# Kernel tuning notes

Hardware: AMD Instinct MI355X
Metric: run time of the kernel (lower is better)

The kernel has to match this reference:

```python
import jax, jax.numpy as jnp
import numpy as np

B, N, H, HEADS = 4, 4096, 256, 8
DEG = 16
E = B * N * DEG  # 262144 edges
DH = H // HEADS


def setup_inputs() -> dict:
    key = jax.random.key(0)
    ks = jax.random.split(key, 8)
    node_states = jax.random.normal(ks[0], (B, N, H), dtype=jnp.float32)
    # edge_indices rows: [batch_idx, target_node, source_node]
    b_idx = jnp.repeat(jnp.arange(B, dtype=jnp.int64), N * DEG)
    tgt = jnp.tile(jnp.repeat(jnp.arange(N, dtype=jnp.int64), DEG), B)
    src = jax.random.randint(ks[1], (E,), 0, N, dtype=jnp.int64)
    edge_indices = jnp.stack([b_idx, tgt, src])  # (3, E)
    s = 1.0 / np.sqrt(H)
    Wq = jax.random.normal(ks[2], (H, H), dtype=jnp.float32) * s
    Wk = jax.random.normal(ks[3], (H, H), dtype=jnp.float32) * s
    Wv = jax.random.normal(ks[4], (H, H), dtype=jnp.float32) * s
    bq = jnp.zeros((H,), dtype=jnp.float32)
    bk = jnp.zeros((H,), dtype=jnp.float32)
    bv = jnp.zeros((H,), dtype=jnp.float32)
    return {"node_states": node_states, "edge_indices": edge_indices,
            "Wq": Wq, "bq": bq, "Wk": Wk, "bk": bk, "Wv": Wv, "bv": bv}


def reference(node_states, edge_indices, Wq, bq, Wk, bk, Wv, bv):
    batch, n_nodes, hidden = node_states.shape
    b_idx, tgt, src = edge_indices[0], edge_indices[1], edge_indices[2]
    num_edges = b_idx.shape[0]

    # Dense Q/K/V projections on nodes (cheap), then per-edge gathers.
    Q = (node_states @ Wq + bq).reshape(batch, n_nodes, HEADS, DH)
    K = (node_states @ Wk + bk).reshape(batch, n_nodes, HEADS, DH)
    V = (node_states @ Wv + bv).reshape(batch, n_nodes, HEADS, DH)

    q_e = Q[b_idx, tgt]  # (E, heads, dh)
    k_e = K[b_idx, src]  # (E, heads, dh)
    scores = jnp.sum(q_e * k_e, axis=-1) / jnp.sqrt(jnp.float32(DH))  # (E, heads)

    # Segment softmax over source nodes, grouped per (batch, target) --
    # mirrors torch.sparse.softmax(logits, dim=-2).
    seg = b_idx * n_nodes + tgt  # (E,)
    num_seg = batch * n_nodes
    m = jax.ops.segment_max(scores, seg, num_segments=num_seg)  # (B*N, heads)
    exp = jnp.exp(scores - m[seg])
    denom = jax.ops.segment_sum(exp, seg, num_segments=num_seg)
    attn = exp / denom[seg]  # (E, heads)

    # Weighted scatter-sum of source values into target nodes
    # (replaces sparse edge_mask @ elwise_prod).
    v_e = V[b_idx, src]  # (E, heads, dh)
    weighted = (attn[..., None] * v_e).reshape(num_edges, hidden)
    out = jax.ops.segment_sum(weighted, seg, num_segments=num_seg)
    return out.reshape(batch, n_nodes, hidden)
```

## Files before the change

kernel.cpp:

```cpp
#include <hip/hip_runtime.h>
#include <hip/hip_bf16.h>

#define BATCH 4
#define NNODES 4096
#define HID 256
#define NHEADS 8
#define DH 32
#define DEG 16
#define NEDGES (BATCH * NNODES * DEG)
#define NROWS (BATCH * NNODES)

typedef __attribute__((ext_vector_type(8))) short short8;
typedef __attribute__((ext_vector_type(8))) unsigned short ushort8;
typedef __attribute__((ext_vector_type(4))) unsigned short u16x4;
typedef __attribute__((ext_vector_type(4))) float f32x4;

static __device__ __forceinline__ unsigned short f2bf(float f) {
  __hip_bfloat16 h = __float2bfloat16(f);
  return *reinterpret_cast<unsigned short*>(&h);
}
static __device__ __forceinline__ float bf2f(unsigned short u) {
  unsigned int v = ((unsigned int)u) << 16;
  return *reinterpret_cast<float*>(&v);
}

#define XBLOCKS 2048
#define WBLOCKS 96
__global__ __launch_bounds__(256) void prep_kernel(
    const float* __restrict__ X,
    const float* __restrict__ Wq, const float* __restrict__ Wk,
    const float* __restrict__ Wv,
    unsigned short* __restrict__ Xb, unsigned short* __restrict__ Wt) {
  const int tid = threadIdx.x;
  if (blockIdx.x < XBLOCKS) {
    const size_t base = (size_t)blockIdx.x * 2048 + (size_t)tid * 8;
    const float4 a = *reinterpret_cast<const float4*>(&X[base]);
    const float4 b = *reinterpret_cast<const float4*>(&X[base + 4]);
    ushort8 o;
    o[0] = f2bf(a.x); o[1] = f2bf(a.y); o[2] = f2bf(a.z); o[3] = f2bf(a.w);
    o[4] = f2bf(b.x); o[5] = f2bf(b.y); o[6] = f2bf(b.z); o[7] = f2bf(b.w);
    *reinterpret_cast<ushort8*>(&Xb[base]) = o;
  } else {
    const int o = (blockIdx.x - XBLOCKS) * 2048 + tid * 8;
    const int mat   = o >> 16;
    const int w     = o & 65535;
    const int strip = w >> 14;
    const int r     = w & 16383;
    const int kk    = r >> 11;
    const int hi    = (r >> 9) & 3;
    const int col   = (r >> 3) & 63;
    const int k0    = kk * 32 + hi * 8;
    const int c     = strip * 64 + col;
    const float* __restrict__ W = (mat == 0) ? Wq : (mat == 1) ? Wk : Wv;
    ushort8 ovec;
    #pragma unroll
    for (int j = 0; j < 8; ++j) {
      ovec[j] = f2bf(W[(size_t)(k0 + j) * HID + c]);
    }
    *reinterpret_cast<ushort8*>(&Wt[o]) = ovec;
  }
}

__global__ __launch_bounds__(256, 4) void qkv_mfma_kernel(
    const unsigned short* __restrict__ Xb, const unsigned short* __restrict__ Wt,
    const float* __restrict__ bq, const float* __restrict__ bk,
    const float* __restrict__ bv,
    float* __restrict__ Qs, unsigned short* __restrict__ Kb,
    unsigned short* __restrict__ Vb) {
  __shared__ unsigned short sW[16384];

  const int tid = threadIdx.x;
  const int s = blockIdx.x >> 8;
  const int chunk = blockIdx.x & 255;
  const int mat = s >> 2;
  const int c0 = (s & 3) * 64;

  const unsigned short* __restrict__ Wsrc = Wt + (size_t)(mat * 4 + (s & 3)) * 16384;
  #pragma unroll
  for (int i = 0; i < 8; ++i) {
    const int e = i * 2048 + tid * 8;
    *reinterpret_cast<ushort8*>(&sW[e]) =
        *reinterpret_cast<const ushort8*>(&Wsrc[e]);
  }

  const int lane = tid & 63;
  const int wv = tid >> 6;
  const int lm = lane & 15;
  const int hi = lane >> 4;
  const int lk = hi * 8;
  const int r0 = chunk * 64 + wv * 16;
  const int row = r0 + lm;

  short8 Af[8];
  #pragma unroll
  for (int kk = 0; kk < 8; ++kk) {
    Af[kk] = *reinterpret_cast<const short8*>(
        &Xb[(size_t)row * 256 + kk * 32 + lk]);
  }

  const float* __restrict__ bias = (mat == 0) ? bq : (mat == 1) ? bk : bv;

  __syncthreads();

  #pragma unroll
  for (int nt = 0; nt < 4; ++nt) {
    short8 Bf[8];
    #pragma unroll
    for (int kk = 0; kk < 8; ++kk) {
      Bf[kk] = *reinterpret_cast<const short8*>(
          &sW[kk * 2048 + hi * 512 + (nt * 16 + lm) * 8]);
    }
    f32x4 acc = {0.f, 0.f, 0.f, 0.f};
    #pragma unroll
    for (int kk = 0; kk < 8; ++kk) {
      acc = __builtin_amdgcn_mfma_f32_16x16x32_bf16(Bf[kk], Af[kk], acc, 0, 0, 0);
    }
    const int col0 = c0 + nt * 16 + hi * 4;
    const float4 b4 = *reinterpret_cast<const float4*>(&bias[col0]);
    if (mat == 0) {
      float4 o;
      o.x = acc[0] + b4.x; o.y = acc[1] + b4.y;
      o.z = acc[2] + b4.z; o.w = acc[3] + b4.w;
      *reinterpret_cast<float4*>(&Qs[(size_t)row * 256 + col0]) = o;
    } else {
      u16x4 o;
      o[0] = f2bf(acc[0] + b4.x); o[1] = f2bf(acc[1] + b4.y);
      o[2] = f2bf(acc[2] + b4.z); o[3] = f2bf(acc[3] + b4.w);
      unsigned short* __restrict__ dst = (mat == 1) ? Kb : Vb;
      *reinterpret_cast<u16x4*>(&dst[(size_t)row * 256 + col0]) = o;
    }
  }
}

__global__ __launch_bounds__(256) void attn_kernel(
    const float* __restrict__ Q, const unsigned short* __restrict__ K,
    const unsigned short* __restrict__ V, const int* __restrict__ edges,
    float* __restrict__ out) {
  __shared__ int s_n[DEG];
  __shared__ float s_q[8 * 36];
  __shared__ float s_sc[DEG][8];
  __shared__ float s_w[DEG][8];

  const int bx = blockIdx.x;
  const int xcd = bx & 7;
  const int g = (xcd >> 1) * NNODES + (((bx >> 3) << 1) | (xcd & 1));
  const int e0 = g * DEG;
  const int tid = threadIdx.x;

  const int b = edges[e0];
  const int qrow = b * NNODES + edges[NEDGES + e0];
  if (tid < DEG) {
    s_n[tid] = b * NNODES + edges[2 * NEDGES + e0 + tid];
  }
  s_q[(tid >> 5) * 36 + (tid & 31)] = Q[(size_t)qrow * HID + tid];
  __syncthreads();

  const int j = tid >> 4;
  const int h = (tid >> 1) & 7;
  const int p = tid & 1;
  const int n1 = s_n[j];
  const unsigned short* __restrict__ krow = &K[(size_t)n1 * HID + h * 32 + p * 16];
  const ushort8 k0 = *reinterpret_cast<const ushort8*>(krow);
  const ushort8 k1 = *reinterpret_cast<const ushort8*>(krow + 8);
  const float* __restrict__ qp = &s_q[h * 36 + p * 16];
  float partial = 0.0f;
  #pragma unroll
  for (int i = 0; i < 8; ++i) partial = fmaf(qp[i], bf2f(k0[i]), partial);
  #pragma unroll
  for (int i = 0; i < 8; ++i) partial = fmaf(qp[8 + i], bf2f(k1[i]), partial);
  partial += __shfl_xor(partial, 1);
  if (p == 0) s_sc[j][h] = partial;
  __syncthreads();

  if (tid < 128) {
    const int tj = tid & 15;
    const int th = tid >> 4;
    const float sc = s_sc[tj][th] * 0.17677669529663687f;
    float mx = sc;
    mx = fmaxf(mx, __shfl_xor(mx, 1));
    mx = fmaxf(mx, __shfl_xor(mx, 2));
    mx = fmaxf(mx, __shfl_xor(mx, 4));
    mx = fmaxf(mx, __shfl_xor(mx, 8));
    const float e = __expf(sc - mx);
    float sum = e;
    sum += __shfl_xor(sum, 1);
    sum += __shfl_xor(sum, 2);
    sum += __shfl_xor(sum, 4);
    sum += __shfl_xor(sum, 8);
    s_w[tj][th] = e / sum;
  }
  __syncthreads();

  const int h3 = tid >> 5;
  float acc = 0.0f;
  #pragma unroll
  for (int jj = 0; jj < DEG; ++jj) {
    acc = fmaf(s_w[jj][h3], bf2f(V[(size_t)s_n[jj] * HID + tid]), acc);
  }
  out[(size_t)qrow * HID + tid] = acc;
}

extern "C" void kernel_launch(void* const* d_in, const int* in_sizes, int n_in,
                              void* d_out, int out_size, void* d_ws, size_t ws_size,
                              hipStream_t stream) {
  const float* X     = (const float*)d_in[0];
  const int*   edges = (const int*)d_in[1];
  const float* Wq    = (const float*)d_in[2];
  const float* bq    = (const float*)d_in[3];
  const float* Wk    = (const float*)d_in[4];
  const float* bk    = (const float*)d_in[5];
  const float* Wv    = (const float*)d_in[6];
  const float* bv    = (const float*)d_in[7];
  float* out = (float*)d_out;

  char* w = (char*)d_ws;
  float*          Qs = (float*)w;                 w += (size_t)NROWS * HID * 4;
  unsigned short* Kb = (unsigned short*)w;        w += (size_t)NROWS * HID * 2;
  unsigned short* Vb = (unsigned short*)w;        w += (size_t)NROWS * HID * 2;
  unsigned short* Xb = (unsigned short*)w;        w += (size_t)NROWS * HID * 2;
  unsigned short* Wt = (unsigned short*)w;

  prep_kernel<<<XBLOCKS + WBLOCKS, 256, 0, stream>>>(X, Wq, Wk, Wv, Xb, Wt);
  qkv_mfma_kernel<<<3072, 256, 0, stream>>>(Xb, Wt, bq, bk, bv, Qs, Kb, Vb);
  attn_kernel<<<NROWS, 256, 0, stream>>>(Qs, Kb, Vb, edges, out);
}
```

Before: 59.67 us.

## Fuse bf16 conversion into QKV GEMM and make attention softmax wave-local

Removes the separate prep kernel: the QKV MFMA kernel now reads fp32 X and W directly, converting them to bf16 in registers and while scattering W into shared memory. This drops one launch and the round trip of bf16 copies of X and W through global memory. The cost is that every block redoes the W conversion and reads fp32 X at twice the bytes. The attention kernel is also remapped so that each wave holds all 16 edges for two heads, letting the softmax run with wave shuffles and cutting two of its three block barriers and the shared-memory staging of Q and scores.

Result: slower. 71.44 us (+19.7%).

```diff
diff --git a/kernel.cpp b/kernel.cpp
--- a/kernel.cpp
+++ b/kernel.cpp
@@ -24,45 +24,10 @@
   return *reinterpret_cast<float*>(&v);
 }
 
-#define XBLOCKS 2048
-#define WBLOCKS 96
-__global__ __launch_bounds__(256) void prep_kernel(
+__global__ __launch_bounds__(256, 4) void qkv_mfma_kernel(
     const float* __restrict__ X,
     const float* __restrict__ Wq, const float* __restrict__ Wk,
     const float* __restrict__ Wv,
-    unsigned short* __restrict__ Xb, unsigned short* __restrict__ Wt) {
-  const int tid = threadIdx.x;
-  if (blockIdx.x < XBLOCKS) {
-    const size_t base = (size_t)blockIdx.x * 2048 + (size_t)tid * 8;
-    const float4 a = *reinterpret_cast<const float4*>(&X[base]);
-    const float4 b = *reinterpret_cast<const float4*>(&X[base + 4]);
-    ushort8 o;
-    o[0] = f2bf(a.x); o[1] = f2bf(a.y); o[2] = f2bf(a.z); o[3] = f2bf(a.w);
-    o[4] = f2bf(b.x); o[5] = f2bf(b.y); o[6] = f2bf(b.z); o[7] = f2bf(b.w);
-    *reinterpret_cast<ushort8*>(&Xb[base]) = o;
-  } else {
-    const int o = (blockIdx.x - XBLOCKS) * 2048 + tid * 8;
-    const int mat   = o >> 16;
-    const int w     = o & 65535;
-    const int strip = w >> 14;
-    const int r     = w & 16383;
-    const int kk    = r >> 11;
-    const int hi    = (r >> 9) & 3;
-    const int col   = (r >> 3) & 63;
-    const int k0    = kk * 32 + hi * 8;
-    const int c     = strip * 64 + col;
-    const float* __restrict__ W = (mat == 0) ? Wq : (mat == 1) ? Wk : Wv;
-    ushort8 ovec;
-    #pragma unroll
-    for (int j = 0; j < 8; ++j) {
-      ovec[j] = f2bf(W[(size_t)(k0 + j) * HID + c]);
-    }
-    *reinterpret_cast<ushort8*>(&Wt[o]) = ovec;
-  }
-}
-
-__global__ __launch_bounds__(256, 4) void qkv_mfma_kernel(
-    const unsigned short* __restrict__ Xb, const unsigned short* __restrict__ Wt,
     const float* __restrict__ bq, const float* __restrict__ bk,
     const float* __restrict__ bv,
     float* __restrict__ Qs, unsigned short* __restrict__ Kb,
@@ -74,13 +39,18 @@
   const int chunk = blockIdx.x & 255;
   const int mat = s >> 2;
   const int c0 = (s & 3) * 64;
-
-  const unsigned short* __restrict__ Wsrc = Wt + (size_t)(mat * 4 + (s & 3)) * 16384;
-  #pragma unroll
-  for (int i = 0; i < 8; ++i) {
-    const int e = i * 2048 + tid * 8;
-    *reinterpret_cast<ushort8*>(&sW[e]) =
-        *reinterpret_cast<const ushort8*>(&Wsrc[e]);
+  const float* __restrict__ W = (mat == 0) ? Wq : (mat == 1) ? Wk : Wv;
+
+  #pragma unroll
+  for (int i = 0; i < 16; ++i) {
+    const int k = i * 16 + (tid >> 4);
+    const int col = (tid & 15) * 4;
+    const float4 w4 = *reinterpret_cast<const float4*>(&W[(size_t)k * HID + c0 + col]);
+    const int base = (k >> 5) * 2048 + ((k >> 3) & 3) * 512 + (k & 7);
+    sW[base + (col + 0) * 8] = f2bf(w4.x);
+    sW[base + (col + 1) * 8] = f2bf(w4.y);
+    sW[base + (col + 2) * 8] = f2bf(w4.z);
+    sW[base + (col + 3) * 8] = f2bf(w4.w);
   }
 
   const int lane = tid & 63;
@@ -88,14 +58,19 @@
   const int lm = lane & 15;
   const int hi = lane >> 4;
   const int lk = hi * 8;
-  const int r0 = chunk * 64 + wv * 16;
-  const int row = r0 + lm;
+  const int row = chunk * 64 + wv * 16 + lm;
 
   short8 Af[8];
   #pragma unroll
   for (int kk = 0; kk < 8; ++kk) {
-    Af[kk] = *reinterpret_cast<const short8*>(
-        &Xb[(size_t)row * 256 + kk * 32 + lk]);
+    const float4 a0 = *reinterpret_cast<const float4*>(&X[(size_t)row * 256 + kk * 32 + lk]);
+    const float4 a1 = *reinterpret_cast<const float4*>(&X[(size_t)row * 256 + kk * 32 + lk + 4]);
+    short8 v;
+    v[0] = (short)f2bf(a0.x); v[1] = (short)f2bf(a0.y);
+    v[2] = (short)f2bf(a0.z); v[3] = (short)f2bf(a0.w);
+    v[4] = (short)f2bf(a1.x); v[5] = (short)f2bf(a1.y);
+    v[6] = (short)f2bf(a1.z); v[7] = (short)f2bf(a1.w);
+    Af[kk] = v;
   }
 
   const float* __restrict__ bias = (mat == 0) ? bq : (mat == 1) ? bk : bv;
@@ -136,10 +111,7 @@
     const float* __restrict__ Q, const unsigned short* __restrict__ K,
     const unsigned short* __restrict__ V, const int* __restrict__ edges,
     float* __restrict__ out) {
-  __shared__ int s_n[DEG];
-  __shared__ float s_q[8 * 36];
-  __shared__ float s_sc[DEG][8];
-  __shared__ float s_w[DEG][8];
+  __shared__ float s_w[DEG * NHEADS];
 
   const int bx = blockIdx.x;
   const int xcd = bx & 7;
@@ -149,53 +121,60 @@
 
   const int b = edges[e0];
   const int qrow = b * NNODES + edges[NEDGES + e0];
-  if (tid < DEG) {
-    s_n[tid] = b * NNODES + edges[2 * NEDGES + e0 + tid];
-  }
-  s_q[(tid >> 5) * 36 + (tid & 31)] = Q[(size_t)qrow * HID + tid];
-  __syncthreads();
-
-  const int j = tid >> 4;
-  const int h = (tid >> 1) & 7;
-  const int p = tid & 1;
-  const int n1 = s_n[j];
-  const unsigned short* __restrict__ krow = &K[(size_t)n1 * HID + h * 32 + p * 16];
-  const ushort8 k0 = *reinterpret_cast<const ushort8*>(krow);
-  const ushort8 k1 = *reinterpret_cast<const ushort8*>(krow + 8);
-  const float* __restrict__ qp = &s_q[h * 36 + p * 16];
-  float partial = 0.0f;
-  #pragma unroll
-  for (int i = 0; i < 8; ++i) partial = fmaf(qp[i], bf2f(k0[i]), partial);
-  #pragma unroll
-  for (int i = 0; i < 8; ++i) partial = fmaf(qp[8 + i], bf2f(k1[i]), partial);
+
+  const int lane = tid & 63;
+  const int wv = tid >> 6;
+  const int j = lane >> 2;
+  const int hh = (lane >> 1) & 1;
+  const int p = lane & 1;
+  const int h = wv * 2 + hh;
+  const int ch0 = h * 32 + p * 16;
+
+  const int nsrc = b * NNODES + edges[2 * NEDGES + e0 + j];
+
+  const float* __restrict__ qp = &Q[(size_t)qrow * HID + ch0];
+  const float4 q0 = *reinterpret_cast<const float4*>(qp);
+  const float4 q1 = *reinterpret_cast<const float4*>(qp + 4);
+  const float4 q2 = *reinterpret_cast<const float4*>(qp + 8);
+  const float4 q3 = *reinterpret_cast<const float4*>(qp + 12);
+  const unsigned short* __restrict__ kp = &K[(size_t)nsrc * HID + ch0];
+  const ushort8 k0 = *reinterpret_cast<const ushort8*>(kp);
+  const ushort8 k1 = *reinterpret_cast<const ushort8*>(kp + 8);
+
+  float partial;
+  partial  = q0.x * bf2f(k0[0]); partial = fmaf(q0.y, bf2f(k0[1]), partial);
+  partial = fmaf(q0.z, bf2f(k0[2]), partial); partial = fmaf(q0.w, bf2f(k0[3]), partial);
+  partial = fmaf(q1.x, bf2f(k0[4]), partial); partial = fmaf(q1.y, bf2f(k0[5]), partial);
+  partial = fmaf(q1.z, bf2f(k0[6]), partial); partial = fmaf(q1.w, bf2f(k0[7]), partial);
+  partial = fmaf(q2.x, bf2f(k1[0]), partial); partial = fmaf(q2.y, bf2f(k1[1]), partial);
+  partial = fmaf(q2.z, bf2f(k1[2]), partial); partial = fmaf(q2.w, bf2f(k1[3]), partial);
+  partial = fmaf(q3.x, bf2f(k1[4]), partial); partial = fmaf(q3.y, bf2f(k1[5]), partial);
+  partial = fmaf(q3.z, bf2f(k1[6]), partial); partial = fmaf(q3.w, bf2f(k1[7]), partial);
+
   partial += __shfl_xor(partial, 1);
-  if (p == 0) s_sc[j][h] = partial;
-  __syncthreads();
-
-  if (tid < 128) {
-    const int tj = tid & 15;
-    const int th = tid >> 4;
-    const float sc = s_sc[tj][th] * 0.17677669529663687f;
-    float mx = sc;
-    mx = fmaxf(mx, __shfl_xor(mx, 1));
-    mx = fmaxf(mx, __shfl_xor(mx, 2));
-    mx = fmaxf(mx, __shfl_xor(mx, 4));
-    mx = fmaxf(mx, __shfl_xor(mx, 8));
-    const float e = __expf(sc - mx);
-    float sum = e;
-    sum += __shfl_xor(sum, 1);
-    sum += __shfl_xor(sum, 2);
-    sum += __shfl_xor(sum, 4);
-    sum += __shfl_xor(sum, 8);
-    s_w[tj][th] = e / sum;
-  }
+  const float sc = partial * 0.17677669529663687f;
+
+  float mx = sc;
+  mx = fmaxf(mx, __shfl_xor(mx, 4));
+  mx = fmaxf(mx, __shfl_xor(mx, 8));
+  mx = fmaxf(mx, __shfl_xor(mx, 16));
+  mx = fmaxf(mx, __shfl_xor(mx, 32));
+  const float e = __expf(sc - mx);
+  float sum = e;
+  sum += __shfl_xor(sum, 4);
+  sum += __shfl_xor(sum, 8);
+  sum += __shfl_xor(sum, 16);
+  sum += __shfl_xor(sum, 32);
+
+  if (p == 0) s_w[j * NHEADS + h] = e / sum;
   __syncthreads();
 
   const int h3 = tid >> 5;
   float acc = 0.0f;
   #pragma unroll
   for (int jj = 0; jj < DEG; ++jj) {
-    acc = fmaf(s_w[jj][h3], bf2f(V[(size_t)s_n[jj] * HID + tid]), acc);
+    const int n = b * NNODES + edges[2 * NEDGES + e0 + jj];
+    acc = fmaf(s_w[jj * NHEADS + h3], bf2f(V[(size_t)n * HID + tid]), acc);
   }
   out[(size_t)qrow * HID + tid] = acc;
 }
@@ -216,11 +195,8 @@
   char* w = (char*)d_ws;
   float*          Qs = (float*)w;                 w += (size_t)NROWS * HID * 4;
   unsigned short* Kb = (unsigned short*)w;        w += (size_t)NROWS * HID * 2;
-  unsigned short* Vb = (unsigned short*)w;        w += (size_t)NROWS * HID * 2;
-  unsigned short* Xb = (unsigned short*)w;        w += (size_t)NROWS * HID * 2;
-  unsigned short* Wt = (unsigned short*)w;
-
-  prep_kernel<<<XBLOCKS + WBLOCKS, 256, 0, stream>>>(X, Wq, Wk, Wv, Xb, Wt);
-  qkv_mfma_kernel<<<3072, 256, 0, stream>>>(Xb, Wt, bq, bk, bv, Qs, Kb, Vb);
+  unsigned short* Vb = (unsigned short*)w;
+
+  qkv_mfma_kernel<<<3072, 256, 0, stream>>>(X, Wq, Wk, Wv, bq, bk, bv, Qs, Kb, Vb);
   attn_kernel<<<NROWS, 256, 0, stream>>>(Qs, Kb, Vb, edges, out);
 }
```
